# Performance work log

Hardware: AMD Instinct MI355X
Metric: run time of the kernel (lower is better)

## Reference

```python
import jax, jax.numpy as jnp
import numpy as np

B, N, D, H = 8, 2048, 32, 4
HD = D // H  # head_dim = 8
LN_EPS = 1e-5


def setup_inputs() -> dict:
    key = jax.random.key(0)
    ks = jax.random.split(key, 6)
    x = jax.random.normal(ks[0], (B, N, D), dtype=jnp.float32)
    adj_raw = jax.random.uniform(ks[1], (N, N), dtype=jnp.float32)
    adj_prior = adj_raw / (adj_raw.sum(axis=-1, keepdims=True) + 1e-8)
    Wqkv = jax.random.normal(ks[2], (D, 3 * D), dtype=jnp.float32) * (1.0 / np.sqrt(D))
    bqkv = jnp.zeros((3 * D,), dtype=jnp.float32)
    Wout = jax.random.normal(ks[3], (D, D), dtype=jnp.float32) * (1.0 / np.sqrt(D))
    bout = jnp.zeros((D,), dtype=jnp.float32)
    gamma = jnp.ones((D,), dtype=jnp.float32)
    beta = jnp.zeros((D,), dtype=jnp.float32)
    geo_weight = jnp.float32(0.3)
    return {"x": x, "adj_prior": adj_prior, "geo_weight": geo_weight,
            "Wqkv": Wqkv, "bqkv": bqkv, "Wout": Wout, "bout": bout,
            "gamma": gamma, "beta": beta}


def reference(x, adj_prior, geo_weight, Wqkv, bqkv, Wout, bout, gamma, beta):
    b, n, d = x.shape
    qkv = x @ Wqkv + bqkv                        # [B,N,3D]
    qkv = qkv.reshape(b, n, 3, H, HD)
    qkv = jnp.transpose(qkv, (2, 0, 3, 1, 4))    # [3,B,H,N,HD]
    q, k, v = qkv[0], qkv[1], qkv[2]
    scores = jnp.einsum('bhnd,bhmd->bhnm', q, k) / jnp.sqrt(jnp.float32(HD))
    blend = jax.nn.sigmoid(geo_weight)
    scores = (1.0 - blend) * scores + blend * adj_prior[None, None] * 5.0
    w = jax.nn.softmax(scores, axis=-1)          # dropout omitted (eval mode)
    out = jnp.einsum('bhnm,bhmd->bhnd', w, v)    # [B,H,N,HD]
    out = jnp.transpose(out, (0, 2, 1, 3)).reshape(b, n, d)
    out = out @ Wout + bout
    res = out + x
    mu = res.mean(axis=-1, keepdims=True)
    var = res.var(axis=-1, keepdims=True)
    return (res - mu) * jax.lax.rsqrt(var + LN_EPS) * gamma + beta
```

## Files before the change

### kernel.cpp

```cpp
#include <hip/hip_runtime.h>


typedef _Float16 f16;
typedef _Float16 f16x2 __attribute__((ext_vector_type(2)));
typedef _Float16 f16x4 __attribute__((ext_vector_type(4)));
typedef _Float16 f16x8 __attribute__((ext_vector_type(8)));
typedef __fp16 h16x2 __attribute__((ext_vector_type(2)));
typedef float f32x4 __attribute__((ext_vector_type(4)));

__global__ __launch_bounds__(256) void prep_kernel(const float* __restrict__ adj,
                                                   const float* __restrict__ gw_p,
                                                   f16* __restrict__ adj16,
                                                   f16* __restrict__ kf_ws,
                                                   f16* __restrict__ vf_ws) {
  const float LOG2E = 1.4426950408889634f;
  float blend = 1.f / (1.f + __expf(-gw_p[0]));
  float c2 = blend * 5.f * LOG2E;
  int gid = blockIdx.x * 256 + threadIdx.x;
  int tile = gid >> 6, lane = gid & 63;
  int qtp = tile >> 7, jt = tile & 127;
  int col = jt * 16 + (lane >> 4) * 4;
  f32x4 v0 = *(const f32x4*)(adj + (size_t)(qtp * 32 + (lane & 15)) * 2048 + col);
  f32x4 v1 = *(const f32x4*)(adj + (size_t)(qtp * 32 + 16 + (lane & 15)) * 2048 + col);
  f16x8 r;
  r[0] = (f16)(c2 * v0[0]); r[1] = (f16)(c2 * v0[1]);
  r[2] = (f16)(c2 * v0[2]); r[3] = (f16)(c2 * v0[3]);
  r[4] = (f16)(c2 * v1[0]); r[5] = (f16)(c2 * v1[1]);
  r[6] = (f16)(c2 * v1[2]); r[7] = (f16)(c2 * v1[3]);
  *(f16x8*)(adj16 + (size_t)gid * 8) = r;
  if (gid < 262144) {
    const f16x4 z = {};
    if (lane >= 32) *(f16x4*)(kf_ws + (size_t)gid * 4) = z;
    int dq = lane & 15;
    if (dq == 8) {
      f16x4 ones = {(f16)1.f, (f16)1.f, (f16)1.f, (f16)1.f};
      *(f16x4*)(vf_ws + (size_t)gid * 4) = ones;
    } else if (dq > 8) {
      *(f16x4*)(vf_ws + (size_t)gid * 4) = z;
    }
  }
}

__global__ __launch_bounds__(256) void qkv_kernel(
    const float* __restrict__ x, const float* __restrict__ Wqkv,
    const float* __restrict__ bqkv, f16* __restrict__ q16,
    f16* __restrict__ kf_ws, f16* __restrict__ vf_ws) {
  __shared__ float Ws[32 * 96];
  __shared__ float bsh[96];
  __shared__ float xs[16 * 32];
  int tid = threadIdx.x;
  for (int i = tid; i < 32 * 96; i += 256) Ws[i] = Wqkv[i];
  if (tid < 96) bsh[tid] = bqkv[tid];
  int rowbase = blockIdx.x * 16;
  for (int i = tid; i < 16 * 32; i += 256) xs[i] = x[rowbase * 32 + i];
  __syncthreads();
#pragma unroll
  for (int e = 0; e < 6; ++e) {
    int idx = tid + e * 256;
    int r = idx / 96, c = idx % 96;
    float acc = bsh[c];
#pragma unroll
    for (int k = 0; k < 32; ++k) acc += xs[r * 32 + k] * Ws[k * 96 + c];
    int nrow = rowbase + r;
    int b = nrow >> 11, n = nrow & 2047;
    int s = c >> 5, h = (c >> 3) & 3, d = c & 7;
    int bh = b * 4 + h;
    int jt = n >> 4, jr = n & 15;
    if (s == 0) {
      q16[((size_t)bh * 2048 + n) * 8 + d] = (f16)acc;
    } else if (s == 1) {
      int lane = ((d >> 2) << 4) | jr;
      kf_ws[(((size_t)bh * 128 + jt) * 64 + lane) * 4 + (d & 3)] = (f16)acc;
    } else {
      int lane = ((jr >> 2) << 4) | d;
      vf_ws[(((size_t)bh * 128 + jt) * 64 + lane) * 4 + (jr & 3)] = (f16)acc;
    }
  }
}

__global__ __launch_bounds__(512, 4) void attn_kernel(
    const f16* __restrict__ q16, const f16* __restrict__ kf_ws,
    const f16* __restrict__ vf_ws, const f16* __restrict__ adj16,
    const float* __restrict__ gw_p, float* __restrict__ attn_ws) {
  int blk = blockIdx.x;
  int bhp = blk & 15, qtq = blk >> 4;
  int tid = threadIdx.x;
  int w = tid >> 6, lane = tid & 63;
  int lq = lane & 15, lh = lane >> 4;
  int bh0 = bhp * 2;

  const float LOG2E = 1.4426950408889634f;
  float blend = 1.f / (1.f + __expf(-gw_p[0]));
  float c1 = (1.f - blend) * 0.35355339059327373f * LOG2E;

  const f16* kp0 = kf_ws + (((size_t)bh0 * 128 + w * 16) * 64 + lane) * 4;
  const f16* kp1 = kp0 + (size_t)128 * 64 * 4;
  const f16* vp0 = vf_ws + (((size_t)bh0 * 128 + w * 16) * 64 + lane) * 4;
  const f16* vp1 = vp0 + (size_t)128 * 64 * 4;
  const f16* ap0 = adj16 + (((size_t)(qtq * 2) * 128 + w * 16) * 64 + lane) * 8;
  const f16* ap1 = ap0 + (size_t)128 * 64 * 8;

  f16x4 qf[2][4];
#pragma unroll
  for (int u = 0; u < 2; ++u)
#pragma unroll
    for (int m = 0; m < 4; ++m) {
      f16x4 t = {};
      if (lane < 32) {
        f16x4 qr = *(const f16x4*)(q16 + ((size_t)(bh0 + u) * 2048 +
                                          (qtq * 4 + m) * 16 + lq) * 8 + lh * 4);
        t[0] = (f16)(c1 * (float)qr[0]); t[1] = (f16)(c1 * (float)qr[1]);
        t[2] = (f16)(c1 * (float)qr[2]); t[3] = (f16)(c1 * (float)qr[3]);
      }
      qf[u][m] = t;
    }

  f32x4 acc[2][4];
#pragma unroll
  for (int u = 0; u < 2; ++u)
#pragma unroll
    for (int m = 0; m < 4; ++m) acc[u][m] = (f32x4){0.f, 0.f, 0.f, 0.f};
  const f32x4 zero4 = {0.f, 0.f, 0.f, 0.f};

#pragma unroll 4
  for (int t = 0; t < 16; ++t) {
    f16x4 kf0 = *(const f16x4*)(kp0 + t * 256);
    f16x4 kf1 = *(const f16x4*)(kp1 + t * 256);
    f16x4 vf0 = *(const f16x4*)(vp0 + t * 256);
    f16x4 vf1 = *(const f16x4*)(vp1 + t * 256);
    f16x8 av0 = *(const f16x8*)(ap0 + t * 512);
    f16x8 av1 = *(const f16x8*)(ap1 + t * 512);
#pragma unroll
    for (int u = 0; u < 2; ++u) {
      f16x4 kfu = u ? kf1 : kf0;
      f16x4 vfu = u ? vf1 : vf0;
#pragma unroll
      for (int m = 0; m < 4; ++m) {
        f32x4 s = __builtin_amdgcn_mfma_f32_16x16x16f16(kfu, qf[u][m], zero4, 0, 0, 0);
        float a0 = (float)((m < 2 ? av0 : av1)[(m & 1) * 4 + 0]);
        float a1 = (float)((m < 2 ? av0 : av1)[(m & 1) * 4 + 1]);
        float a2 = (float)((m < 2 ? av0 : av1)[(m & 1) * 4 + 2]);
        float a3 = (float)((m < 2 ? av0 : av1)[(m & 1) * 4 + 3]);
        float e0 = __builtin_amdgcn_exp2f(s[0] + a0);
        float e1 = __builtin_amdgcn_exp2f(s[1] + a1);
        float e2 = __builtin_amdgcn_exp2f(s[2] + a2);
        float e3 = __builtin_amdgcn_exp2f(s[3] + a3);
        h16x2 p01 = __builtin_amdgcn_cvt_pkrtz(e0, e1);
        h16x2 p23 = __builtin_amdgcn_cvt_pkrtz(e2, e3);
        f16x4 pa;
        pa[0] = (f16)(float)p01[0]; pa[1] = (f16)(float)p01[1];
        pa[2] = (f16)(float)p23[0]; pa[3] = (f16)(float)p23[1];
        acc[u][m] = __builtin_amdgcn_mfma_f32_16x16x16f16(pa, vfu, acc[u][m], 0, 0, 0);
      }
    }
  }

  __shared__ f32x4 mlds[8][8][64];
#pragma unroll
  for (int u = 0; u < 2; ++u)
#pragma unroll
    for (int m = 0; m < 4; ++m) mlds[w][u * 4 + m][lane] = acc[u][m];
  __syncthreads();
  int p = w;
  f32x4 sum = mlds[0][p][lane];
#pragma unroll
  for (int s = 1; s < 8; ++s) {
    f32x4 o = mlds[s][p][lane];
    sum[0] += o[0]; sum[1] += o[1]; sum[2] += o[2]; sum[3] += o[3];
  }
  int dsrc = (lane & 48) | 8;
  float d0 = __shfl(sum[0], dsrc);
  float d1 = __shfl(sum[1], dsrc);
  float d2 = __shfl(sum[2], dsrc);
  float d3 = __shfl(sum[3], dsrc);
  if (lq < 8) {
    int bh = bh0 + (p >> 2);
    int b = bh >> 2, h = bh & 3;
    int qt0 = (qtq * 4 + (p & 3)) * 16;
    size_t base = ((size_t)b * 2048 + qt0 + lh * 4) * 32 + h * 8 + lq;
    attn_ws[base]      = sum[0] / d0;
    attn_ws[base + 32] = sum[1] / d1;
    attn_ws[base + 64] = sum[2] / d2;
    attn_ws[base + 96] = sum[3] / d3;
  }
}

__global__ __launch_bounds__(256) void out_ln_kernel(
    const float* __restrict__ attn_ws, const float* __restrict__ x,
    const float* __restrict__ Wout, const float* __restrict__ bout,
    const float* __restrict__ gamma, const float* __restrict__ beta,
    float* __restrict__ out) {
  __shared__ float Ws[32 * 32];
  __shared__ float bs[32], gs[32], bts[32];
  int tid = threadIdx.x;
  for (int i = tid; i < 1024; i += 256) Ws[i] = Wout[i];
  if (tid < 32) { bs[tid] = bout[tid]; gs[tid] = gamma[tid]; bts[tid] = beta[tid]; }
  __syncthreads();
  int row = blockIdx.x * 8 + (tid >> 5);
  int d = tid & 31;
  const float* ar = attn_ws + (size_t)row * 32;
  float acc = bs[d];
#pragma unroll
  for (int k = 0; k < 32; ++k) acc += ar[k] * Ws[k * 32 + d];
  float res = acc + x[(size_t)row * 32 + d];
  float s1 = res, s2 = res * res;
#pragma unroll
  for (int off = 16; off >= 1; off >>= 1) {
    s1 += __shfl_xor(s1, off);
    s2 += __shfl_xor(s2, off);
  }
  float mu = s1 * 0.03125f;
  float var = s2 * 0.03125f - mu * mu;
  float r = rsqrtf(var + 1e-5f);
  out[(size_t)row * 32 + d] = (res - mu) * r * gs[d] + bts[d];
}

extern "C" void kernel_launch(void* const* d_in, const int* in_sizes, int n_in,
                              void* d_out, int out_size, void* d_ws, size_t ws_size,
                              hipStream_t stream) {
  const float* x     = (const float*)d_in[0];
  const float* adj   = (const float*)d_in[1];
  const float* gw    = (const float*)d_in[2];
  const float* Wqkv  = (const float*)d_in[3];
  const float* bqkv  = (const float*)d_in[4];
  const float* Wout  = (const float*)d_in[5];
  const float* bout  = (const float*)d_in[6];
  const float* gamma = (const float*)d_in[7];
  const float* beta  = (const float*)d_in[8];
  float* out = (float*)d_out;

  char* wsb = (char*)d_ws;
  f16* q16       = (f16*)wsb;
  f16* kf_ws     = (f16*)(wsb + (1 << 20));
  f16* vf_ws     = (f16*)(wsb + (3 << 20));
  f16* adj16     = (f16*)(wsb + (5 << 20));
  float* attn_ws = (float*)(wsb + (13 << 20));

  qkv_kernel<<<1024, 256, 0, stream>>>(x, Wqkv, bqkv, q16, kf_ws, vf_ws);
  prep_kernel<<<2048, 256, 0, stream>>>(adj, gw, adj16, kf_ws, vf_ws);
  attn_kernel<<<512, 512, 0, stream>>>(q16, kf_ws, vf_ws, adj16, gw, attn_ws);
  out_ln_kernel<<<2048, 256, 0, stream>>>(attn_ws, x, Wout, bout, gamma, beta, out);
}
```

Baseline: 54.75 us.

## Merge prep and QKV kernels, process four heads per attention block

Folds the adjacency prep and the QKV projection into one launch, and moves the Q pre-scaling into the projection so the attention kernel no longer does it. Each attention block now handles four (batch, head) pairs instead of two, so every adjacency tile it loads is reused across more heads and the grid halves. The cross-wave reduction becomes a tree reduction through shared memory, and launch bounds drop to two blocks. The larger per-wave register footprint and the extra barriers may cut occupancy and latency hiding.

```diff
diff --git a/kernel.cpp b/kernel.cpp
--- a/kernel.cpp
+++ b/kernel.cpp
@@ -2,145 +2,139 @@
 
 
 typedef _Float16 f16;
-typedef _Float16 f16x2 __attribute__((ext_vector_type(2)));
 typedef _Float16 f16x4 __attribute__((ext_vector_type(4)));
 typedef _Float16 f16x8 __attribute__((ext_vector_type(8)));
 typedef __fp16 h16x2 __attribute__((ext_vector_type(2)));
 typedef float f32x4 __attribute__((ext_vector_type(4)));
 
-__global__ __launch_bounds__(256) void prep_kernel(const float* __restrict__ adj,
-                                                   const float* __restrict__ gw_p,
-                                                   f16* __restrict__ adj16,
-                                                   f16* __restrict__ kf_ws,
-                                                   f16* __restrict__ vf_ws) {
+__global__ __launch_bounds__(256) void prep_qkv_kernel(
+    const float* __restrict__ x, const float* __restrict__ Wqkv,
+    const float* __restrict__ bqkv, const float* __restrict__ adj,
+    const float* __restrict__ gw_p, f16* __restrict__ q16,
+    f16* __restrict__ kf_ws, f16* __restrict__ vf_ws,
+    f16* __restrict__ adj16) {
   const float LOG2E = 1.4426950408889634f;
   float blend = 1.f / (1.f + __expf(-gw_p[0]));
-  float c2 = blend * 5.f * LOG2E;
-  int gid = blockIdx.x * 256 + threadIdx.x;
-  int tile = gid >> 6, lane = gid & 63;
-  int qtp = tile >> 7, jt = tile & 127;
-  int col = jt * 16 + (lane >> 4) * 4;
-  f32x4 v0 = *(const f32x4*)(adj + (size_t)(qtp * 32 + (lane & 15)) * 2048 + col);
-  f32x4 v1 = *(const f32x4*)(adj + (size_t)(qtp * 32 + 16 + (lane & 15)) * 2048 + col);
-  f16x8 r;
-  r[0] = (f16)(c2 * v0[0]); r[1] = (f16)(c2 * v0[1]);
-  r[2] = (f16)(c2 * v0[2]); r[3] = (f16)(c2 * v0[3]);
-  r[4] = (f16)(c2 * v1[0]); r[5] = (f16)(c2 * v1[1]);
-  r[6] = (f16)(c2 * v1[2]); r[7] = (f16)(c2 * v1[3]);
-  *(f16x8*)(adj16 + (size_t)gid * 8) = r;
-  if (gid < 262144) {
-    const f16x4 z = {};
-    if (lane >= 32) *(f16x4*)(kf_ws + (size_t)gid * 4) = z;
-    int dq = lane & 15;
-    if (dq == 8) {
-      f16x4 ones = {(f16)1.f, (f16)1.f, (f16)1.f, (f16)1.f};
-      *(f16x4*)(vf_ws + (size_t)gid * 4) = ones;
-    } else if (dq > 8) {
-      *(f16x4*)(vf_ws + (size_t)gid * 4) = z;
-    }
-  }
-}
-
-__global__ __launch_bounds__(256) void qkv_kernel(
-    const float* __restrict__ x, const float* __restrict__ Wqkv,
-    const float* __restrict__ bqkv, f16* __restrict__ q16,
-    f16* __restrict__ kf_ws, f16* __restrict__ vf_ws) {
+  int tid = threadIdx.x;
   __shared__ float Ws[32 * 96];
   __shared__ float bsh[96];
   __shared__ float xs[16 * 32];
-  int tid = threadIdx.x;
-  for (int i = tid; i < 32 * 96; i += 256) Ws[i] = Wqkv[i];
-  if (tid < 96) bsh[tid] = bqkv[tid];
-  int rowbase = blockIdx.x * 16;
-  for (int i = tid; i < 16 * 32; i += 256) xs[i] = x[rowbase * 32 + i];
-  __syncthreads();
-#pragma unroll
-  for (int e = 0; e < 6; ++e) {
-    int idx = tid + e * 256;
-    int r = idx / 96, c = idx % 96;
-    float acc = bsh[c];
-#pragma unroll
-    for (int k = 0; k < 32; ++k) acc += xs[r * 32 + k] * Ws[k * 96 + c];
-    int nrow = rowbase + r;
-    int b = nrow >> 11, n = nrow & 2047;
-    int s = c >> 5, h = (c >> 3) & 3, d = c & 7;
-    int bh = b * 4 + h;
-    int jt = n >> 4, jr = n & 15;
-    if (s == 0) {
-      q16[((size_t)bh * 2048 + n) * 8 + d] = (f16)acc;
-    } else if (s == 1) {
-      int lane = ((d >> 2) << 4) | jr;
-      kf_ws[(((size_t)bh * 128 + jt) * 64 + lane) * 4 + (d & 3)] = (f16)acc;
-    } else {
-      int lane = ((jr >> 2) << 4) | d;
-      vf_ws[(((size_t)bh * 128 + jt) * 64 + lane) * 4 + (jr & 3)] = (f16)acc;
-    }
-  }
-}
-
-__global__ __launch_bounds__(512, 4) void attn_kernel(
+
+  if (blockIdx.x < 2048) {
+    float c2 = blend * 5.f * LOG2E;
+    int gid = blockIdx.x * 256 + tid;
+    int tile = gid >> 6, lane = gid & 63;
+    int qtp = tile >> 7, jt = tile & 127;
+    int col = jt * 16 + (lane >> 4) * 4;
+    f32x4 v0 = *(const f32x4*)(adj + (size_t)(qtp * 32 + (lane & 15)) * 2048 + col);
+    f32x4 v1 = *(const f32x4*)(adj + (size_t)(qtp * 32 + 16 + (lane & 15)) * 2048 + col);
+    f16x8 r;
+    r[0] = (f16)(c2 * v0[0]); r[1] = (f16)(c2 * v0[1]);
+    r[2] = (f16)(c2 * v0[2]); r[3] = (f16)(c2 * v0[3]);
+    r[4] = (f16)(c2 * v1[0]); r[5] = (f16)(c2 * v1[1]);
+    r[6] = (f16)(c2 * v1[2]); r[7] = (f16)(c2 * v1[3]);
+    *(f16x8*)(adj16 + (size_t)gid * 8) = r;
+    if (gid < 262144) {
+      const f16x4 z = {};
+      if (lane >= 32) *(f16x4*)(kf_ws + (size_t)gid * 4) = z;
+      int dq = lane & 15;
+      if (dq == 8) {
+        f16x4 ones = {(f16)1.f, (f16)1.f, (f16)1.f, (f16)1.f};
+        *(f16x4*)(vf_ws + (size_t)gid * 4) = ones;
+      } else if (dq > 8) {
+        *(f16x4*)(vf_ws + (size_t)gid * 4) = z;
+      }
+    }
+  } else {
+    float c1 = (1.f - blend) * 0.35355339059327373f * LOG2E;
+    int blk = blockIdx.x - 2048;
+    for (int i = tid; i < 32 * 96; i += 256) Ws[i] = Wqkv[i];
+    if (tid < 96) bsh[tid] = bqkv[tid];
+    int rowbase = blk * 16;
+    for (int i = tid; i < 16 * 32; i += 256) xs[i] = x[rowbase * 32 + i];
+    __syncthreads();
+#pragma unroll
+    for (int e = 0; e < 6; ++e) {
+      int idx = tid + e * 256;
+      int r = idx / 96, c = idx % 96;
+      float acc = bsh[c];
+#pragma unroll
+      for (int k = 0; k < 32; ++k) acc += xs[r * 32 + k] * Ws[k * 96 + c];
+      int nrow = rowbase + r;
+      int b = nrow >> 11, n = nrow & 2047;
+      int s = c >> 5, h = (c >> 3) & 3, d = c & 7;
+      int bh = b * 4 + h;
+      int jt = n >> 4, jr = n & 15;
+      if (s == 0) {
+        q16[((size_t)bh * 2048 + n) * 8 + d] = (f16)(acc * c1);
+      } else if (s == 1) {
+        int lane = ((d >> 2) << 4) | jr;
+        kf_ws[(((size_t)bh * 128 + jt) * 64 + lane) * 4 + (d & 3)] = (f16)acc;
+      } else {
+        int lane = ((jr >> 2) << 4) | d;
+        vf_ws[(((size_t)bh * 128 + jt) * 64 + lane) * 4 + (jr & 3)] = (f16)acc;
+      }
+    }
+  }
+}
+
+__global__ __launch_bounds__(512, 2) void attn_kernel(
     const f16* __restrict__ q16, const f16* __restrict__ kf_ws,
     const f16* __restrict__ vf_ws, const f16* __restrict__ adj16,
-    const float* __restrict__ gw_p, float* __restrict__ attn_ws) {
+    float* __restrict__ attn_ws) {
   int blk = blockIdx.x;
-  int bhp = blk & 15, qtq = blk >> 4;
+  int bhg = blk & 7;
+  int qtg = blk >> 3;
   int tid = threadIdx.x;
   int w = tid >> 6, lane = tid & 63;
   int lq = lane & 15, lh = lane >> 4;
-  int bh0 = bhp * 2;
-
-  const float LOG2E = 1.4426950408889634f;
-  float blend = 1.f / (1.f + __expf(-gw_p[0]));
-  float c1 = (1.f - blend) * 0.35355339059327373f * LOG2E;
-
-  const f16* kp0 = kf_ws + (((size_t)bh0 * 128 + w * 16) * 64 + lane) * 4;
-  const f16* kp1 = kp0 + (size_t)128 * 64 * 4;
-  const f16* vp0 = vf_ws + (((size_t)bh0 * 128 + w * 16) * 64 + lane) * 4;
-  const f16* vp1 = vp0 + (size_t)128 * 64 * 4;
-  const f16* ap0 = adj16 + (((size_t)(qtq * 2) * 128 + w * 16) * 64 + lane) * 8;
+  int bh0 = bhg * 4;
+  int jt0 = w * 16;
+
+  const f16* kp = kf_ws + (((size_t)bh0 * 128 + jt0) * 64 + lane) * 4;
+  const f16* vp = vf_ws + (((size_t)bh0 * 128 + jt0) * 64 + lane) * 4;
+  int qtp0 = qtg * 2;
+  const f16* ap0 = adj16 + (((size_t)qtp0 * 128 + jt0) * 64 + lane) * 8;
   const f16* ap1 = ap0 + (size_t)128 * 64 * 8;
 
-  f16x4 qf[2][4];
-#pragma unroll
-  for (int u = 0; u < 2; ++u)
+  f16x4 qf[4][4];
+#pragma unroll
+  for (int u = 0; u < 4; ++u)
 #pragma unroll
     for (int m = 0; m < 4; ++m) {
       f16x4 t = {};
-      if (lane < 32) {
-        f16x4 qr = *(const f16x4*)(q16 + ((size_t)(bh0 + u) * 2048 +
-                                          (qtq * 4 + m) * 16 + lq) * 8 + lh * 4);
-        t[0] = (f16)(c1 * (float)qr[0]); t[1] = (f16)(c1 * (float)qr[1]);
-        t[2] = (f16)(c1 * (float)qr[2]); t[3] = (f16)(c1 * (float)qr[3]);
-      }
+      if (lane < 32)
+        t = *(const f16x4*)(q16 + ((size_t)(bh0 + u) * 2048 +
+                                   (qtg * 4 + m) * 16 + lq) * 8 + lh * 4);
       qf[u][m] = t;
     }
 
-  f32x4 acc[2][4];
-#pragma unroll
-  for (int u = 0; u < 2; ++u)
+  f32x4 acc[4][4];
+#pragma unroll
+  for (int u = 0; u < 4; ++u)
 #pragma unroll
     for (int m = 0; m < 4; ++m) acc[u][m] = (f32x4){0.f, 0.f, 0.f, 0.f};
   const f32x4 zero4 = {0.f, 0.f, 0.f, 0.f};
 
-#pragma unroll 4
+#pragma unroll 2
   for (int t = 0; t < 16; ++t) {
-    f16x4 kf0 = *(const f16x4*)(kp0 + t * 256);
-    f16x4 kf1 = *(const f16x4*)(kp1 + t * 256);
-    f16x4 vf0 = *(const f16x4*)(vp0 + t * 256);
-    f16x4 vf1 = *(const f16x4*)(vp1 + t * 256);
+    f16x4 kf[4], vf[4];
+#pragma unroll
+    for (int u = 0; u < 4; ++u) {
+      kf[u] = *(const f16x4*)(kp + u * 32768 + t * 256);
+      vf[u] = *(const f16x4*)(vp + u * 32768 + t * 256);
+    }
     f16x8 av0 = *(const f16x8*)(ap0 + t * 512);
     f16x8 av1 = *(const f16x8*)(ap1 + t * 512);
 #pragma unroll
-    for (int u = 0; u < 2; ++u) {
-      f16x4 kfu = u ? kf1 : kf0;
-      f16x4 vfu = u ? vf1 : vf0;
-#pragma unroll
-      for (int m = 0; m < 4; ++m) {
-        f32x4 s = __builtin_amdgcn_mfma_f32_16x16x16f16(kfu, qf[u][m], zero4, 0, 0, 0);
-        float a0 = (float)((m < 2 ? av0 : av1)[(m & 1) * 4 + 0]);
-        float a1 = (float)((m < 2 ? av0 : av1)[(m & 1) * 4 + 1]);
-        float a2 = (float)((m < 2 ? av0 : av1)[(m & 1) * 4 + 2]);
-        float a3 = (float)((m < 2 ? av0 : av1)[(m & 1) * 4 + 3]);
+    for (int u = 0; u < 4; ++u) {
+#pragma unroll
+      for (int m = 0; m < 4; ++m) {
+        f32x4 s = __builtin_amdgcn_mfma_f32_16x16x16f16(kf[u], qf[u][m], zero4, 0, 0, 0);
+        float a0 = (float)((m < 2) ? av0[(m & 1) * 4 + 0] : av1[(m & 1) * 4 + 0]);
+        float a1 = (float)((m < 2) ? av0[(m & 1) * 4 + 1] : av1[(m & 1) * 4 + 1]);
+        float a2 = (float)((m < 2) ? av0[(m & 1) * 4 + 2] : av1[(m & 1) * 4 + 2]);
+        float a3 = (float)((m < 2) ? av0[(m & 1) * 4 + 3] : av1[(m & 1) * 4 + 3]);
         float e0 = __builtin_amdgcn_exp2f(s[0] + a0);
         float e1 = __builtin_amdgcn_exp2f(s[1] + a1);
         float e2 = __builtin_amdgcn_exp2f(s[2] + a2);
@@ -150,38 +144,86 @@
         f16x4 pa;
         pa[0] = (f16)(float)p01[0]; pa[1] = (f16)(float)p01[1];
         pa[2] = (f16)(float)p23[0]; pa[3] = (f16)(float)p23[1];
-        acc[u][m] = __builtin_amdgcn_mfma_f32_16x16x16f16(pa, vfu, acc[u][m], 0, 0, 0);
-      }
-    }
-  }
-
-  __shared__ f32x4 mlds[8][8][64];
-#pragma unroll
-  for (int u = 0; u < 2; ++u)
-#pragma unroll
-    for (int m = 0; m < 4; ++m) mlds[w][u * 4 + m][lane] = acc[u][m];
-  __syncthreads();
-  int p = w;
-  f32x4 sum = mlds[0][p][lane];
-#pragma unroll
-  for (int s = 1; s < 8; ++s) {
-    f32x4 o = mlds[s][p][lane];
-    sum[0] += o[0]; sum[1] += o[1]; sum[2] += o[2]; sum[3] += o[3];
-  }
-  int dsrc = (lane & 48) | 8;
-  float d0 = __shfl(sum[0], dsrc);
-  float d1 = __shfl(sum[1], dsrc);
-  float d2 = __shfl(sum[2], dsrc);
-  float d3 = __shfl(sum[3], dsrc);
-  if (lq < 8) {
-    int bh = bh0 + (p >> 2);
-    int b = bh >> 2, h = bh & 3;
-    int qt0 = (qtq * 4 + (p & 3)) * 16;
-    size_t base = ((size_t)b * 2048 + qt0 + lh * 4) * 32 + h * 8 + lq;
-    attn_ws[base]      = sum[0] / d0;
-    attn_ws[base + 32] = sum[1] / d1;
-    attn_ws[base + 64] = sum[2] / d2;
-    attn_ws[base + 96] = sum[3] / d3;
+        acc[u][m] = __builtin_amdgcn_mfma_f32_16x16x16f16(pa, vf[u], acc[u][m], 0, 0, 0);
+      }
+    }
+  }
+
+  __shared__ f32x4 mlds[4][16][64];
+  if (w & 1) {
+#pragma unroll
+    for (int u = 0; u < 4; ++u)
+#pragma unroll
+      for (int m = 0; m < 4; ++m) mlds[w >> 1][u * 4 + m][lane] = acc[u][m];
+  }
+  __syncthreads();
+  if (!(w & 1)) {
+#pragma unroll
+    for (int u = 0; u < 4; ++u)
+#pragma unroll
+      for (int m = 0; m < 4; ++m) {
+        f32x4 o = mlds[w >> 1][u * 4 + m][lane];
+        acc[u][m][0] += o[0]; acc[u][m][1] += o[1];
+        acc[u][m][2] += o[2]; acc[u][m][3] += o[3];
+      }
+  }
+  __syncthreads();
+  if (w == 2 || w == 6) {
+#pragma unroll
+    for (int u = 0; u < 4; ++u)
+#pragma unroll
+      for (int m = 0; m < 4; ++m) mlds[(w >> 2)][u * 4 + m][lane] = acc[u][m];
+  }
+  __syncthreads();
+  if (w == 0 || w == 4) {
+#pragma unroll
+    for (int u = 0; u < 4; ++u)
+#pragma unroll
+      for (int m = 0; m < 4; ++m) {
+        f32x4 o = mlds[(w >> 2)][u * 4 + m][lane];
+        acc[u][m][0] += o[0]; acc[u][m][1] += o[1];
+        acc[u][m][2] += o[2]; acc[u][m][3] += o[3];
+      }
+  }
+  __syncthreads();
+  if (w == 4) {
+#pragma unroll
+    for (int u = 0; u < 4; ++u)
+#pragma unroll
+      for (int m = 0; m < 4; ++m) mlds[2][u * 4 + m][lane] = acc[u][m];
+  }
+  __syncthreads();
+  if (w == 0) {
+#pragma unroll
+    for (int u = 0; u < 4; ++u)
+#pragma unroll
+      for (int m = 0; m < 4; ++m) {
+        f32x4 o = mlds[2][u * 4 + m][lane];
+        acc[u][m][0] += o[0]; acc[u][m][1] += o[1];
+        acc[u][m][2] += o[2]; acc[u][m][3] += o[3];
+      }
+    int dsrc = (lane & 48) | 8;
+#pragma unroll
+    for (int u = 0; u < 4; ++u) {
+      int bh = bh0 + u;
+      int b = bh >> 2, h = bh & 3;
+#pragma unroll
+      for (int m = 0; m < 4; ++m) {
+        f32x4 s = acc[u][m];
+        float d0 = __shfl(s[0], dsrc);
+        float d1 = __shfl(s[1], dsrc);
+        float d2 = __shfl(s[2], dsrc);
+        float d3 = __shfl(s[3], dsrc);
+        if (lq < 8) {
+          int qt = qtg * 4 + m;
+          size_t base = ((size_t)b * 2048 + qt * 16 + lh * 4) * 32 + h * 8 + lq;
+          attn_ws[base]      = s[0] / d0;
+          attn_ws[base + 32] = s[1] / d1;
+          attn_ws[base + 64] = s[2] / d2;
+          attn_ws[base + 96] = s[3] / d3;
+        }
+      }
+    }
   }
 }
 
@@ -236,8 +278,8 @@
   f16* adj16     = (f16*)(wsb + (5 << 20));
   float* attn_ws = (float*)(wsb + (13 << 20));
 
-  qkv_kernel<<<1024, 256, 0, stream>>>(x, Wqkv, bqkv, q16, kf_ws, vf_ws);
-  prep_kernel<<<2048, 256, 0, stream>>>(adj, gw, adj16, kf_ws, vf_ws);
-  attn_kernel<<<512, 512, 0, stream>>>(q16, kf_ws, vf_ws, adj16, gw, attn_ws);
+  prep_qkv_kernel<<<3072, 256, 0, stream>>>(x, Wqkv, bqkv, adj, gw,
+                                            q16, kf_ws, vf_ws, adj16);
+  attn_kernel<<<256, 512, 0, stream>>>(q16, kf_ws, vf_ws, adj16, attn_ws);
   out_ln_kernel<<<2048, 256, 0, stream>>>(attn_ws, x, Wout, bout, gamma, beta, out);
 }
```

Measured after the change: 57.44 us. +4.9%, slower.

## Merge prep and QKV kernels, precompute exp of adjacency prior, remap attention blocks

Applied to the files above, without the earlier changes.

Merges the QKV projection and the adjacency/workspace prep into one launch, with block ranges split between the two jobs. The adjacency prior is stored as exp2 of its scaled value, so the attention inner loop computes exp2 of the score alone and multiplies by the stored factor in packed fp16. This moves the per-element add out of the hot loop. The Q scale is folded into the projection, and attention blocks are reordered so that blocks sharing an adjacency tile run closer together. The risk is extra fp16 rounding from multiplying exponentials, though prior values stay small because rows are normalized.

```diff
diff --git a/kernel.cpp b/kernel.cpp
--- a/kernel.cpp
+++ b/kernel.cpp
@@ -2,78 +2,83 @@
 
 
 typedef _Float16 f16;
-typedef _Float16 f16x2 __attribute__((ext_vector_type(2)));
 typedef _Float16 f16x4 __attribute__((ext_vector_type(4)));
 typedef _Float16 f16x8 __attribute__((ext_vector_type(8)));
 typedef __fp16 h16x2 __attribute__((ext_vector_type(2)));
+typedef __fp16 h16x8 __attribute__((ext_vector_type(8)));
 typedef float f32x4 __attribute__((ext_vector_type(4)));
 
-__global__ __launch_bounds__(256) void prep_kernel(const float* __restrict__ adj,
-                                                   const float* __restrict__ gw_p,
-                                                   f16* __restrict__ adj16,
-                                                   f16* __restrict__ kf_ws,
-                                                   f16* __restrict__ vf_ws) {
+__global__ __launch_bounds__(256) void prep_qkv_kernel(
+    const float* __restrict__ x, const float* __restrict__ Wqkv,
+    const float* __restrict__ bqkv, const float* __restrict__ adj,
+    const float* __restrict__ gw_p, f16* __restrict__ q16,
+    f16* __restrict__ kf_ws, f16* __restrict__ vf_ws,
+    f16* __restrict__ adj16) {
   const float LOG2E = 1.4426950408889634f;
   float blend = 1.f / (1.f + __expf(-gw_p[0]));
-  float c2 = blend * 5.f * LOG2E;
-  int gid = blockIdx.x * 256 + threadIdx.x;
-  int tile = gid >> 6, lane = gid & 63;
-  int qtp = tile >> 7, jt = tile & 127;
-  int col = jt * 16 + (lane >> 4) * 4;
-  f32x4 v0 = *(const f32x4*)(adj + (size_t)(qtp * 32 + (lane & 15)) * 2048 + col);
-  f32x4 v1 = *(const f32x4*)(adj + (size_t)(qtp * 32 + 16 + (lane & 15)) * 2048 + col);
-  f16x8 r;
-  r[0] = (f16)(c2 * v0[0]); r[1] = (f16)(c2 * v0[1]);
-  r[2] = (f16)(c2 * v0[2]); r[3] = (f16)(c2 * v0[3]);
-  r[4] = (f16)(c2 * v1[0]); r[5] = (f16)(c2 * v1[1]);
-  r[6] = (f16)(c2 * v1[2]); r[7] = (f16)(c2 * v1[3]);
-  *(f16x8*)(adj16 + (size_t)gid * 8) = r;
-  if (gid < 262144) {
-    const f16x4 z = {};
-    if (lane >= 32) *(f16x4*)(kf_ws + (size_t)gid * 4) = z;
-    int dq = lane & 15;
-    if (dq == 8) {
-      f16x4 ones = {(f16)1.f, (f16)1.f, (f16)1.f, (f16)1.f};
-      *(f16x4*)(vf_ws + (size_t)gid * 4) = ones;
-    } else if (dq > 8) {
-      *(f16x4*)(vf_ws + (size_t)gid * 4) = z;
-    }
-  }
-}
-
-__global__ __launch_bounds__(256) void qkv_kernel(
-    const float* __restrict__ x, const float* __restrict__ Wqkv,
-    const float* __restrict__ bqkv, f16* __restrict__ q16,
-    f16* __restrict__ kf_ws, f16* __restrict__ vf_ws) {
+  int tid = threadIdx.x;
   __shared__ float Ws[32 * 96];
   __shared__ float bsh[96];
   __shared__ float xs[16 * 32];
-  int tid = threadIdx.x;
-  for (int i = tid; i < 32 * 96; i += 256) Ws[i] = Wqkv[i];
-  if (tid < 96) bsh[tid] = bqkv[tid];
-  int rowbase = blockIdx.x * 16;
-  for (int i = tid; i < 16 * 32; i += 256) xs[i] = x[rowbase * 32 + i];
-  __syncthreads();
-#pragma unroll
-  for (int e = 0; e < 6; ++e) {
-    int idx = tid + e * 256;
-    int r = idx / 96, c = idx % 96;
-    float acc = bsh[c];
-#pragma unroll
-    for (int k = 0; k < 32; ++k) acc += xs[r * 32 + k] * Ws[k * 96 + c];
-    int nrow = rowbase + r;
-    int b = nrow >> 11, n = nrow & 2047;
-    int s = c >> 5, h = (c >> 3) & 3, d = c & 7;
-    int bh = b * 4 + h;
-    int jt = n >> 4, jr = n & 15;
-    if (s == 0) {
-      q16[((size_t)bh * 2048 + n) * 8 + d] = (f16)acc;
-    } else if (s == 1) {
-      int lane = ((d >> 2) << 4) | jr;
-      kf_ws[(((size_t)bh * 128 + jt) * 64 + lane) * 4 + (d & 3)] = (f16)acc;
-    } else {
-      int lane = ((jr >> 2) << 4) | d;
-      vf_ws[(((size_t)bh * 128 + jt) * 64 + lane) * 4 + (jr & 3)] = (f16)acc;
+
+  if (blockIdx.x < 2048) {
+    float c2 = blend * 5.f * LOG2E;
+    int gid = blockIdx.x * 256 + tid;
+    int tile = gid >> 6, lane = gid & 63;
+    int qtp = tile >> 7, jt = tile & 127;
+    int col = jt * 16 + (lane >> 4) * 4;
+    f32x4 v0 = *(const f32x4*)(adj + (size_t)(qtp * 32 + (lane & 15)) * 2048 + col);
+    f32x4 v1 = *(const f32x4*)(adj + (size_t)(qtp * 32 + 16 + (lane & 15)) * 2048 + col);
+    f16x8 r;
+    r[0] = (f16)__builtin_amdgcn_exp2f(c2 * v0[0]);
+    r[1] = (f16)__builtin_amdgcn_exp2f(c2 * v0[1]);
+    r[2] = (f16)__builtin_amdgcn_exp2f(c2 * v0[2]);
+    r[3] = (f16)__builtin_amdgcn_exp2f(c2 * v0[3]);
+    r[4] = (f16)__builtin_amdgcn_exp2f(c2 * v1[0]);
+    r[5] = (f16)__builtin_amdgcn_exp2f(c2 * v1[1]);
+    r[6] = (f16)__builtin_amdgcn_exp2f(c2 * v1[2]);
+    r[7] = (f16)__builtin_amdgcn_exp2f(c2 * v1[3]);
+    *(f16x8*)(adj16 + (size_t)gid * 8) = r;
+    if (gid < 262144) {
+      const f16x4 z = {};
+      if (lane >= 32) *(f16x4*)(kf_ws + (size_t)gid * 4) = z;
+      int dq = lane & 15;
+      if (dq == 8) {
+        f16x4 ones = {(f16)1.f, (f16)1.f, (f16)1.f, (f16)1.f};
+        *(f16x4*)(vf_ws + (size_t)gid * 4) = ones;
+      } else if (dq > 8) {
+        *(f16x4*)(vf_ws + (size_t)gid * 4) = z;
+      }
+    }
+  } else {
+    float c1 = (1.f - blend) * 0.35355339059327373f * LOG2E;
+    int blk = blockIdx.x - 2048;
+    for (int i = tid; i < 32 * 96; i += 256) Ws[i] = Wqkv[i];
+    if (tid < 96) bsh[tid] = bqkv[tid];
+    int rowbase = blk * 16;
+    for (int i = tid; i < 16 * 32; i += 256) xs[i] = x[rowbase * 32 + i];
+    __syncthreads();
+#pragma unroll
+    for (int e = 0; e < 6; ++e) {
+      int idx = tid + e * 256;
+      int r = idx / 96, c = idx % 96;
+      float acc = bsh[c];
+#pragma unroll
+      for (int k = 0; k < 32; ++k) acc += xs[r * 32 + k] * Ws[k * 96 + c];
+      int nrow = rowbase + r;
+      int b = nrow >> 11, n = nrow & 2047;
+      int s = c >> 5, h = (c >> 3) & 3, d = c & 7;
+      int bh = b * 4 + h;
+      int jt = n >> 4, jr = n & 15;
+      if (s == 0) {
+        q16[((size_t)bh * 2048 + n) * 8 + d] = (f16)(acc * c1);
+      } else if (s == 1) {
+        int lane = ((d >> 2) << 4) | jr;
+        kf_ws[(((size_t)bh * 128 + jt) * 64 + lane) * 4 + (d & 3)] = (f16)acc;
+      } else {
+        int lane = ((jr >> 2) << 4) | d;
+        vf_ws[(((size_t)bh * 128 + jt) * 64 + lane) * 4 + (jr & 3)] = (f16)acc;
+      }
     }
   }
 }
@@ -81,23 +86,23 @@
 __global__ __launch_bounds__(512, 4) void attn_kernel(
     const f16* __restrict__ q16, const f16* __restrict__ kf_ws,
     const f16* __restrict__ vf_ws, const f16* __restrict__ adj16,
-    const float* __restrict__ gw_p, float* __restrict__ attn_ws) {
+    float* __restrict__ attn_ws) {
   int blk = blockIdx.x;
-  int bhp = blk & 15, qtq = blk >> 4;
+  int chunk = blk & 7;
+  int within = blk >> 3;
+  int bhp = within & 15;
+  int qtq = (chunk << 2) | (within >> 4);
   int tid = threadIdx.x;
   int w = tid >> 6, lane = tid & 63;
   int lq = lane & 15, lh = lane >> 4;
   int bh0 = bhp * 2;
-
-  const float LOG2E = 1.4426950408889634f;
-  float blend = 1.f / (1.f + __expf(-gw_p[0]));
-  float c1 = (1.f - blend) * 0.35355339059327373f * LOG2E;
-
-  const f16* kp0 = kf_ws + (((size_t)bh0 * 128 + w * 16) * 64 + lane) * 4;
+  int jt0 = w * 16;
+
+  const f16* kp0 = kf_ws + (((size_t)bh0 * 128 + jt0) * 64 + lane) * 4;
   const f16* kp1 = kp0 + (size_t)128 * 64 * 4;
-  const f16* vp0 = vf_ws + (((size_t)bh0 * 128 + w * 16) * 64 + lane) * 4;
+  const f16* vp0 = vf_ws + (((size_t)bh0 * 128 + jt0) * 64 + lane) * 4;
   const f16* vp1 = vp0 + (size_t)128 * 64 * 4;
-  const f16* ap0 = adj16 + (((size_t)(qtq * 2) * 128 + w * 16) * 64 + lane) * 8;
+  const f16* ap0 = adj16 + (((size_t)(qtq * 2) * 128 + jt0) * 64 + lane) * 8;
   const f16* ap1 = ap0 + (size_t)128 * 64 * 8;
 
   f16x4 qf[2][4];
@@ -106,12 +111,9 @@
 #pragma unroll
     for (int m = 0; m < 4; ++m) {
       f16x4 t = {};
-      if (lane < 32) {
-        f16x4 qr = *(const f16x4*)(q16 + ((size_t)(bh0 + u) * 2048 +
-                                          (qtq * 4 + m) * 16 + lq) * 8 + lh * 4);
-        t[0] = (f16)(c1 * (float)qr[0]); t[1] = (f16)(c1 * (float)qr[1]);
-        t[2] = (f16)(c1 * (float)qr[2]); t[3] = (f16)(c1 * (float)qr[3]);
-      }
+      if (lane < 32)
+        t = *(const f16x4*)(q16 + ((size_t)(bh0 + u) * 2048 +
+                                   (qtq * 4 + m) * 16 + lq) * 8 + lh * 4);
       qf[u][m] = t;
     }
 
@@ -128,8 +130,8 @@
     f16x4 kf1 = *(const f16x4*)(kp1 + t * 256);
     f16x4 vf0 = *(const f16x4*)(vp0 + t * 256);
     f16x4 vf1 = *(const f16x4*)(vp1 + t * 256);
-    f16x8 av0 = *(const f16x8*)(ap0 + t * 512);
-    f16x8 av1 = *(const f16x8*)(ap1 + t * 512);
+    h16x8 av0 = *(const h16x8*)(ap0 + t * 512);
+    h16x8 av1 = *(const h16x8*)(ap1 + t * 512);
 #pragma unroll
     for (int u = 0; u < 2; ++u) {
       f16x4 kfu = u ? kf1 : kf0;
@@ -137,16 +139,18 @@
 #pragma unroll
       for (int m = 0; m < 4; ++m) {
         f32x4 s = __builtin_amdgcn_mfma_f32_16x16x16f16(kfu, qf[u][m], zero4, 0, 0, 0);
-        float a0 = (float)((m < 2 ? av0 : av1)[(m & 1) * 4 + 0]);
-        float a1 = (float)((m < 2 ? av0 : av1)[(m & 1) * 4 + 1]);
-        float a2 = (float)((m < 2 ? av0 : av1)[(m & 1) * 4 + 2]);
-        float a3 = (float)((m < 2 ? av0 : av1)[(m & 1) * 4 + 3]);
-        float e0 = __builtin_amdgcn_exp2f(s[0] + a0);
-        float e1 = __builtin_amdgcn_exp2f(s[1] + a1);
-        float e2 = __builtin_amdgcn_exp2f(s[2] + a2);
-        float e3 = __builtin_amdgcn_exp2f(s[3] + a3);
+        h16x8 av = (m < 2) ? av0 : av1;
+        int b4 = (m & 1) * 4;
+        float e0 = __builtin_amdgcn_exp2f(s[0]);
+        float e1 = __builtin_amdgcn_exp2f(s[1]);
+        float e2 = __builtin_amdgcn_exp2f(s[2]);
+        float e3 = __builtin_amdgcn_exp2f(s[3]);
         h16x2 p01 = __builtin_amdgcn_cvt_pkrtz(e0, e1);
         h16x2 p23 = __builtin_amdgcn_cvt_pkrtz(e2, e3);
+        h16x2 ea01 = {av[b4 + 0], av[b4 + 1]};
+        h16x2 ea23 = {av[b4 + 2], av[b4 + 3]};
+        p01 *= ea01;
+        p23 *= ea23;
         f16x4 pa;
         pa[0] = (f16)(float)p01[0]; pa[1] = (f16)(float)p01[1];
         pa[2] = (f16)(float)p23[0]; pa[3] = (f16)(float)p23[1];
@@ -236,8 +240,8 @@
   f16* adj16     = (f16*)(wsb + (5 << 20));
   float* attn_ws = (float*)(wsb + (13 << 20));
 
-  qkv_kernel<<<1024, 256, 0, stream>>>(x, Wqkv, bqkv, q16, kf_ws, vf_ws);
-  prep_kernel<<<2048, 256, 0, stream>>>(adj, gw, adj16, kf_ws, vf_ws);
-  attn_kernel<<<512, 512, 0, stream>>>(q16, kf_ws, vf_ws, adj16, gw, attn_ws);
+  prep_qkv_kernel<<<3072, 256, 0, stream>>>(x, Wqkv, bqkv, adj, gw,
+                                            q16, kf_ws, vf_ws, adj16);
+  attn_kernel<<<512, 512, 0, stream>>>(q16, kf_ws, vf_ws, adj16, attn_ws);
   out_ln_kernel<<<2048, 256, 0, stream>>>(attn_ws, x, Wout, bout, gamma, beta, out);
 }
```

After: 47.08 us. -14.0%, faster.
